# Kernel optimization log

Measured on AMD Instinct MI355X. Metric: run time of the kernel, lower is better.

## Reference

```python
import jax, jax.numpy as jnp
import numpy as np

N_NODES = 40000
N_EDGES = 640000
NFEAT = 256
NHID = 128


def setup_inputs() -> dict:
    key = jax.random.key(0)
    k1, k2, k3, k4 = jax.random.split(key, 4)
    x = jax.random.normal(k1, (N_NODES, NFEAT), dtype=jnp.float32)
    edge_index = jax.random.randint(k2, (2, N_EDGES), 0, N_NODES, dtype=jnp.int64)
    edge_weight = jax.random.uniform(k3, (N_EDGES,), dtype=jnp.float32)
    # Glorot-style init for the GraphConvolution weight, zero bias
    W = jax.random.normal(k4, (NFEAT, NHID), dtype=jnp.float32) * (1.0 / np.sqrt(NFEAT))
    b = jnp.zeros((NHID,), dtype=jnp.float32)
    return {"x": x, "edge_index": edge_index, "edge_weight": edge_weight, "W": W, "b": b}


def reference(x, edge_index, edge_weight, W, b):
    # GraphConvolution: support = x @ W ; out = spmm(adj, support) + b ; relu
    support = x @ W                                   # [N, nhid]
    src, dst = edge_index[0], edge_index[1]
    msgs = support[src] * edge_weight[:, None]        # [E, nhid] gathered messages
    agg = jax.ops.segment_sum(msgs, dst, num_segments=N_NODES)  # [N, nhid]
    return jax.nn.relu(agg + b)
```

## Files before the change

kernel.cpp:

```cpp
#include <hip/hip_runtime.h>

#define NNODES 40000
#define NEDGES 640000
#define NFEAT  256
#define NHID   128
#define CAP    48

#define SUP_OFF 0u
#define CUR_OFF 10240000u
#define WT_OFF  10400000u
#define BKT_OFF 10465536u
#define WS_NEEDED (BKT_OFF + (size_t)NNODES * CAP * 4)

#define GEMM_BLOCKS (NNODES / 64)
#define FILL_BLOCKS (NEDGES / 1024)

typedef float floatx4 __attribute__((ext_vector_type(4)));
typedef __bf16 bf16x8 __attribute__((ext_vector_type(8)));
typedef unsigned short ushort8 __attribute__((ext_vector_type(8)));
union BfFrag { ushort8 s; bf16x8 b; };

__device__ __forceinline__ unsigned short f2bf(float f) {
    unsigned int u = __float_as_uint(f);
    u = (u + 0x7FFFu + ((u >> 16) & 1u)) >> 16;
    return (unsigned short)u;
}

__device__ __forceinline__ float4 bf4(unsigned int lo, unsigned int hi) {
    float4 v;
    v.x = __uint_as_float(lo << 16);
    v.y = __uint_as_float(lo & 0xFFFF0000u);
    v.z = __uint_as_float(hi << 16);
    v.w = __uint_as_float(hi & 0xFFFF0000u);
    return v;
}

__global__ __launch_bounds__(256) void setup_wt_cur(const float* __restrict__ W,
                                                    unsigned short* __restrict__ Wt,
                                                    int* __restrict__ cursor) {
    const int i = blockIdx.x * 256 + threadIdx.x;
    if (i < NNODES) cursor[i] = 0;
    if (i < NFEAT * NHID) {
        const int h = i >> 8;
        const int k = i & 255;
        Wt[i] = f2bf(W[k * NHID + h]);
    }
}

__global__ __launch_bounds__(256) void gemm_fill(const float* __restrict__ x,
                                                 const unsigned short* __restrict__ Wt,
                                                 unsigned short* __restrict__ support,
                                                 const int* __restrict__ ei,
                                                 const float* __restrict__ ew,
                                                 int* __restrict__ cursor,
                                                 unsigned int* __restrict__ bucket) {
    const int tid = threadIdx.x;

    if (blockIdx.x >= GEMM_BLOCKS) {
        const int base = (blockIdx.x - GEMM_BLOCKS) * 1024 + tid;

        int src[4], dst[4];
        float w[4];
        #pragma unroll
        for (int j = 0; j < 4; j++) {
            const int e = base + j * 256;
            src[j] = ei[e];
            dst[j] = ei[NEDGES + e];
            w[j]   = ew[e];
        }

        int pos[4];
        #pragma unroll
        for (int j = 0; j < 4; j++)
            pos[j] = atomicAdd(&cursor[dst[j]], 1);

        #pragma unroll
        for (int j = 0; j < 4; j++) {
            const unsigned int entry =
                ((unsigned int)f2bf(w[j]) << 16) | (unsigned int)src[j];
            if (pos[j] < CAP)
                bucket[(size_t)dst[j] * CAP + pos[j]] = entry;
        }
        return;
    }

    const int lane = tid & 63;
    const int wv   = tid >> 6;
    const int m    = lane & 15;
    const int quad = lane >> 4;
    const int node = blockIdx.x * 64 + wv * 16 + m;

    BfFrag afrag[8];
    const float* xrow = x + (size_t)node * NFEAT + quad * 8;
    #pragma unroll
    for (int ks = 0; ks < 8; ks++) {
        float4 f0 = *(const float4*)(xrow + ks * 32);
        float4 f1 = *(const float4*)(xrow + ks * 32 + 4);
        afrag[ks].s[0] = f2bf(f0.x); afrag[ks].s[1] = f2bf(f0.y);
        afrag[ks].s[2] = f2bf(f0.z); afrag[ks].s[3] = f2bf(f0.w);
        afrag[ks].s[4] = f2bf(f1.x); afrag[ks].s[5] = f2bf(f1.y);
        afrag[ks].s[6] = f2bf(f1.z); afrag[ks].s[7] = f2bf(f1.w);
    }

    floatx4 acc[8];
    #pragma unroll
    for (int nt = 0; nt < 8; nt++) acc[nt] = (floatx4){0.f, 0.f, 0.f, 0.f};

    #pragma unroll
    for (int nt = 0; nt < 8; nt++) {
        const unsigned short* wrow = Wt + (size_t)(nt * 16 + m) * NFEAT + quad * 8;
        #pragma unroll
        for (int ks = 0; ks < 8; ks++) {
            BfFrag bfrag;
            bfrag.s = *(const ushort8*)(wrow + ks * 32);
            acc[nt] = __builtin_amdgcn_mfma_f32_16x16x32_bf16(afrag[ks].b, bfrag.b,
                                                              acc[nt], 0, 0, 0);
        }
    }

    const int row0 = blockIdx.x * 64 + wv * 16 + quad * 4;
    #pragma unroll
    for (int nt = 0; nt < 8; nt++) {
        #pragma unroll
        for (int r = 0; r < 4; r++) {
            support[(size_t)(row0 + r) * NHID + nt * 16 + m] = f2bf(acc[nt][r]);
        }
    }
}

__global__ __launch_bounds__(256) void gather_csr(const int* __restrict__ cursor,
                                                  const unsigned int* __restrict__ bucket,
                                                  const unsigned short* __restrict__ support,
                                                  const float* __restrict__ b,
                                                  float* __restrict__ out) {
    const int node = blockIdx.x * 4 + (threadIdx.x >> 6);
    const int lane = threadIdx.x & 63;
    const int q    = lane >> 4;
    const int ql   = lane & 15;

    int cnt = cursor[node];
    if (cnt > CAP) cnt = CAP;
    const unsigned int* bkt  = bucket + (size_t)node * CAP;
    const uint4*        sup4 = (const uint4*)support;

    float4 lo0 = make_float4(0.f, 0.f, 0.f, 0.f), lo1 = lo0, lo2 = lo0, lo3 = lo0;
    float4 hi0 = lo0, hi1 = lo0, hi2 = lo0, hi3 = lo0;

    int i = 0;
    for (; i + 16 <= cnt; i += 16) {
        unsigned int e0 = bkt[i + 0  + q];
        unsigned int e1 = bkt[i + 4  + q];
        unsigned int e2 = bkt[i + 8  + q];
        unsigned int e3 = bkt[i + 12 + q];
        uint4 u0 = sup4[(size_t)(e0 & 0xFFFFu) * 16 + ql];
        uint4 u1 = sup4[(size_t)(e1 & 0xFFFFu) * 16 + ql];
        uint4 u2 = sup4[(size_t)(e2 & 0xFFFFu) * 16 + ql];
        uint4 u3 = sup4[(size_t)(e3 & 0xFFFFu) * 16 + ql];
        float w0 = __uint_as_float(e0 & 0xFFFF0000u);
        float w1 = __uint_as_float(e1 & 0xFFFF0000u);
        float w2 = __uint_as_float(e2 & 0xFFFF0000u);
        float w3 = __uint_as_float(e3 & 0xFFFF0000u);
        float4 vl0 = bf4(u0.x, u0.y), vh0 = bf4(u0.z, u0.w);
        float4 vl1 = bf4(u1.x, u1.y), vh1 = bf4(u1.z, u1.w);
        float4 vl2 = bf4(u2.x, u2.y), vh2 = bf4(u2.z, u2.w);
        float4 vl3 = bf4(u3.x, u3.y), vh3 = bf4(u3.z, u3.w);
        lo0.x = fmaf(w0, vl0.x, lo0.x); lo0.y = fmaf(w0, vl0.y, lo0.y);
        lo0.z = fmaf(w0, vl0.z, lo0.z); lo0.w = fmaf(w0, vl0.w, lo0.w);
        hi0.x = fmaf(w0, vh0.x, hi0.x); hi0.y = fmaf(w0, vh0.y, hi0.y);
        hi0.z = fmaf(w0, vh0.z, hi0.z); hi0.w = fmaf(w0, vh0.w, hi0.w);
        lo1.x = fmaf(w1, vl1.x, lo1.x); lo1.y = fmaf(w1, vl1.y, lo1.y);
        lo1.z = fmaf(w1, vl1.z, lo1.z); lo1.w = fmaf(w1, vl1.w, lo1.w);
        hi1.x = fmaf(w1, vh1.x, hi1.x); hi1.y = fmaf(w1, vh1.y, hi1.y);
        hi1.z = fmaf(w1, vh1.z, hi1.z); hi1.w = fmaf(w1, vh1.w, hi1.w);
        lo2.x = fmaf(w2, vl2.x, lo2.x); lo2.y = fmaf(w2, vl2.y, lo2.y);
        lo2.z = fmaf(w2, vl2.z, lo2.z); lo2.w = fmaf(w2, vl2.w, lo2.w);
        hi2.x = fmaf(w2, vh2.x, hi2.x); hi2.y = fmaf(w2, vh2.y, hi2.y);
        hi2.z = fmaf(w2, vh2.z, hi2.z); hi2.w = fmaf(w2, vh2.w, hi2.w);
        lo3.x = fmaf(w3, vl3.x, lo3.x); lo3.y = fmaf(w3, vl3.y, lo3.y);
        lo3.z = fmaf(w3, vl3.z, lo3.z); lo3.w = fmaf(w3, vl3.w, lo3.w);
        hi3.x = fmaf(w3, vh3.x, hi3.x); hi3.y = fmaf(w3, vh3.y, hi3.y);
        hi3.z = fmaf(w3, vh3.z, hi3.z); hi3.w = fmaf(w3, vh3.w, hi3.w);
    }

    if (i < cnt) {
        #pragma unroll
        for (int j = 0; j < 4; j++) {
            int e = i + 4 * j + q;
            bool valid = e < cnt;
            unsigned int ent = bkt[valid ? e : 0];
            float w = valid ? __uint_as_float(ent & 0xFFFF0000u) : 0.f;
            uint4 u = sup4[(size_t)(ent & 0xFFFFu) * 16 + ql];
            float4 vl = bf4(u.x, u.y), vh = bf4(u.z, u.w);
            lo0.x = fmaf(w, vl.x, lo0.x); lo0.y = fmaf(w, vl.y, lo0.y);
            lo0.z = fmaf(w, vl.z, lo0.z); lo0.w = fmaf(w, vl.w, lo0.w);
            hi0.x = fmaf(w, vh.x, hi0.x); hi0.y = fmaf(w, vh.y, hi0.y);
            hi0.z = fmaf(w, vh.z, hi0.z); hi0.w = fmaf(w, vh.w, hi0.w);
        }
    }

    float4 L, H;
    L.x = (lo0.x + lo1.x) + (lo2.x + lo3.x);
    L.y = (lo0.y + lo1.y) + (lo2.y + lo3.y);
    L.z = (lo0.z + lo1.z) + (lo2.z + lo3.z);
    L.w = (lo0.w + lo1.w) + (lo2.w + lo3.w);
    H.x = (hi0.x + hi1.x) + (hi2.x + hi3.x);
    H.y = (hi0.y + hi1.y) + (hi2.y + hi3.y);
    H.z = (hi0.z + hi1.z) + (hi2.z + hi3.z);
    H.w = (hi0.w + hi1.w) + (hi2.w + hi3.w);

    L.x += __shfl_xor(L.x, 16); L.y += __shfl_xor(L.y, 16);
    L.z += __shfl_xor(L.z, 16); L.w += __shfl_xor(L.w, 16);
    H.x += __shfl_xor(H.x, 16); H.y += __shfl_xor(H.y, 16);
    H.z += __shfl_xor(H.z, 16); H.w += __shfl_xor(H.w, 16);
    L.x += __shfl_xor(L.x, 32); L.y += __shfl_xor(L.y, 32);
    L.z += __shfl_xor(L.z, 32); L.w += __shfl_xor(L.w, 32);
    H.x += __shfl_xor(H.x, 32); H.y += __shfl_xor(H.y, 32);
    H.z += __shfl_xor(H.z, 32); H.w += __shfl_xor(H.w, 32);

    if (q == 0) {
        const float4* b4p = (const float4*)b;
        float4 bl = b4p[ql * 2], bh = b4p[ql * 2 + 1];
        L.x = fmaxf(L.x + bl.x, 0.f); L.y = fmaxf(L.y + bl.y, 0.f);
        L.z = fmaxf(L.z + bl.z, 0.f); L.w = fmaxf(L.w + bl.w, 0.f);
        H.x = fmaxf(H.x + bh.x, 0.f); H.y = fmaxf(H.y + bh.y, 0.f);
        H.z = fmaxf(H.z + bh.z, 0.f); H.w = fmaxf(H.w + bh.w, 0.f);
        float4* o4 = (float4*)out + (size_t)node * (NHID / 4);
        o4[ql * 2]     = L;
        o4[ql * 2 + 1] = H;
    }
}

__global__ __launch_bounds__(256) void gemm_xw(const float* __restrict__ x,
                                               const float* __restrict__ W,
                                               float* __restrict__ support) {
    __shared__ float xs[64 * NFEAT];
    const int tid   = threadIdx.x;
    const int node0 = blockIdx.x * 64;

    const float4* xg  = (const float4*)(x + (size_t)node0 * NFEAT);
    float4*       xs4 = (float4*)xs;
    #pragma unroll
    for (int i = tid; i < 64 * (NFEAT / 4); i += 256) xs4[i] = xg[i];
    __syncthreads();

    const int hg = tid & 31;
    const int ng = tid >> 5;
    const float4* W4 = (const float4*)W;

    float4 acc[8];
    #pragma unroll
    for (int n = 0; n < 8; n++) acc[n] = make_float4(0.f, 0.f, 0.f, 0.f);

    #pragma unroll 4
    for (int k = 0; k < NFEAT; k++) {
        float4 w = W4[k * (NHID / 4) + hg];
        #pragma unroll
        for (int n = 0; n < 8; n++) {
            float xv = xs[(ng * 8 + n) * NFEAT + k];
            acc[n].x = fmaf(xv, w.x, acc[n].x);
            acc[n].y = fmaf(xv, w.y, acc[n].y);
            acc[n].z = fmaf(xv, w.z, acc[n].z);
            acc[n].w = fmaf(xv, w.w, acc[n].w);
        }
    }

    float4* out4 = (float4*)support;
    #pragma unroll
    for (int n = 0; n < 8; n++)
        out4[(size_t)(node0 + ng * 8 + n) * (NHID / 4) + hg] = acc[n];
}

__global__ __launch_bounds__(256) void scatter_edges(const int* __restrict__ ei,
                                                     const float* __restrict__ ew,
                                                     const float* __restrict__ support,
                                                     float* __restrict__ out) {
    const int tid  = threadIdx.x;
    const int lane = tid & 31;
    const int e    = blockIdx.x * 8 + (tid >> 5);
    const int   src = ei[e];
    const int   dst = ei[NEDGES + e];
    const float w   = ew[e];
    const float4* s4 = (const float4*)support;
    float4 v = s4[(size_t)src * (NHID / 4) + lane];
    float* o = out + (size_t)dst * NHID + lane * 4;
    atomicAdd(o + 0, v.x * w);
    atomicAdd(o + 1, v.y * w);
    atomicAdd(o + 2, v.z * w);
    atomicAdd(o + 3, v.w * w);
}

__global__ __launch_bounds__(256) void finalize(float* __restrict__ out,
                                                const float* __restrict__ b) {
    const int i = blockIdx.x * 256 + threadIdx.x;
    float4*       o4 = (float4*)out;
    const float4* b4 = (const float4*)b;
    float4 v  = o4[i];
    float4 bb = b4[i & 31];
    v.x = fmaxf(v.x + bb.x, 0.f);
    v.y = fmaxf(v.y + bb.y, 0.f);
    v.z = fmaxf(v.z + bb.z, 0.f);
    v.w = fmaxf(v.w + bb.w, 0.f);
    o4[i] = v;
}

extern "C" void kernel_launch(void* const* d_in, const int* in_sizes, int n_in,
                              void* d_out, int out_size, void* d_ws, size_t ws_size,
                              hipStream_t stream) {
    const float* x  = (const float*)d_in[0];
    const int*   ei = (const int*)d_in[1];
    const float* ew = (const float*)d_in[2];
    const float* W  = (const float*)d_in[3];
    const float* b  = (const float*)d_in[4];
    float*       out = (float*)d_out;

    char* ws = (char*)d_ws;

    if (ws_size >= WS_NEEDED) {
        unsigned short* support = (unsigned short*)(ws + SUP_OFF);
        int*            cursor  = (int*)(ws + CUR_OFF);
        unsigned short* Wt      = (unsigned short*)(ws + WT_OFF);
        unsigned int*   bucket  = (unsigned int*)(ws + BKT_OFF);

        setup_wt_cur<<<160, 256, 0, stream>>>(W, Wt, cursor);
        gemm_fill<<<GEMM_BLOCKS + FILL_BLOCKS, 256, 0, stream>>>(
            x, Wt, support, ei, ew, cursor, bucket);
        gather_csr<<<NNODES / 4, 256, 0, stream>>>(cursor, bucket, support, b, out);
    } else {
        float* support = (float*)(ws + SUP_OFF);
        gemm_xw<<<NNODES / 64, 256, 0, stream>>>(x, W, support);
        hipMemsetAsync(d_out, 0, (size_t)out_size * sizeof(float), stream);
        scatter_edges<<<NEDGES / 8, 256, 0, stream>>>(ei, ew, support, out);
        finalize<<<out_size / 4 / 256, 256, 0, stream>>>(out, b);
    }
}
```

Before: 156.6 us.

## Partition bucket-fill atomics into 8 node classes and launch fill blocks first

The edge-bucketing part of the fused GEMM+fill kernel is restructured. Each fill block now handles one of 8 node classes (dst & 7) over a slice of edges, and the cursor array is re-laid out so each class owns a contiguous region. The goal is to localize atomic traffic, likely so it stays within one XCD/L2 slice, and the fill blocks are scheduled ahead of the GEMM blocks. In exchange, every fill block reads 8x more edge data (each edge is read by all 8 class blocks), and the gather kernel looks up cursors through a remapped index.

```diff
diff --git a/kernel.cpp b/kernel.cpp
--- a/kernel.cpp
+++ b/kernel.cpp
@@ -13,7 +13,10 @@
 #define WS_NEEDED (BKT_OFF + (size_t)NNODES * CAP * 4)
 
 #define GEMM_BLOCKS (NNODES / 64)
-#define FILL_BLOCKS (NEDGES / 1024)
+#define FILLB   1000
+#define SLICES  (FILLB / 8)
+#define EPSL    (NEDGES / SLICES)
+#define NPERP   (NNODES / 8)
 
 typedef float floatx4 __attribute__((ext_vector_type(4)));
 typedef __bf16 bf16x8 __attribute__((ext_vector_type(8)));
@@ -25,6 +28,8 @@
     u = (u + 0x7FFFu + ((u >> 16) & 1u)) >> 16;
     return (unsigned short)u;
 }
+
+__device__ __forceinline__ int cidx(int n) { return (n & 7) * NPERP + (n >> 3); }
 
 __device__ __forceinline__ float4 bf4(unsigned int lo, unsigned int hi) {
     float4 v;
@@ -56,39 +61,50 @@
                                                  unsigned int* __restrict__ bucket) {
     const int tid = threadIdx.x;
 
-    if (blockIdx.x >= GEMM_BLOCKS) {
-        const int base = (blockIdx.x - GEMM_BLOCKS) * 1024 + tid;
-
-        int src[4], dst[4];
-        float w[4];
-        #pragma unroll
-        for (int j = 0; j < 4; j++) {
-            const int e = base + j * 256;
-            src[j] = ei[e];
-            dst[j] = ei[NEDGES + e];
-            w[j]   = ew[e];
-        }
-
-        int pos[4];
-        #pragma unroll
-        for (int j = 0; j < 4; j++)
-            pos[j] = atomicAdd(&cursor[dst[j]], 1);
-
-        #pragma unroll
-        for (int j = 0; j < 4; j++) {
-            const unsigned int entry =
-                ((unsigned int)f2bf(w[j]) << 16) | (unsigned int)src[j];
-            if (pos[j] < CAP)
-                bucket[(size_t)dst[j] * CAP + pos[j]] = entry;
+    if (blockIdx.x < FILLB) {
+        const int p = blockIdx.x & 7;
+        const int s = blockIdx.x >> 3;
+        int* __restrict__ curp = cursor + p * NPERP;
+        const int base = s * EPSL + tid;
+
+        #pragma unroll 1
+        for (int bq = 0; bq < EPSL / 1024; bq++) {
+            int src[4], dst[4];
+            float w[4];
+            #pragma unroll
+            for (int j = 0; j < 4; j++) {
+                const int e = base + bq * 1024 + j * 256;
+                src[j] = ei[e];
+                dst[j] = ei[NEDGES + e];
+                w[j]   = ew[e];
+            }
+
+            bool act[4];
+            int pos[4];
+            #pragma unroll
+            for (int j = 0; j < 4; j++) {
+                act[j] = (dst[j] & 7) == p;
+                pos[j] = act[j] ? atomicAdd(&curp[dst[j] >> 3], 1) : CAP;
+            }
+
+            #pragma unroll
+            for (int j = 0; j < 4; j++) {
+                if (act[j] && pos[j] < CAP) {
+                    const unsigned int entry =
+                        ((unsigned int)f2bf(w[j]) << 16) | (unsigned int)src[j];
+                    bucket[(size_t)dst[j] * CAP + pos[j]] = entry;
+                }
+            }
         }
         return;
     }
 
+    const int gb   = blockIdx.x - FILLB;
     const int lane = tid & 63;
     const int wv   = tid >> 6;
     const int m    = lane & 15;
     const int quad = lane >> 4;
-    const int node = blockIdx.x * 64 + wv * 16 + m;
+    const int node = gb * 64 + wv * 16 + m;
 
     BfFrag afrag[8];
     const float* xrow = x + (size_t)node * NFEAT + quad * 8;
@@ -118,7 +134,7 @@
         }
     }
 
-    const int row0 = blockIdx.x * 64 + wv * 16 + quad * 4;
+    const int row0 = gb * 64 + wv * 16 + quad * 4;
     #pragma unroll
     for (int nt = 0; nt < 8; nt++) {
         #pragma unroll
@@ -138,7 +154,7 @@
     const int q    = lane >> 4;
     const int ql   = lane & 15;
 
-    int cnt = cursor[node];
+    int cnt = cursor[cidx(node)];
     if (cnt > CAP) cnt = CAP;
     const unsigned int* bkt  = bucket + (size_t)node * CAP;
     const uint4*        sup4 = (const uint4*)support;
@@ -322,7 +338,7 @@
         unsigned int*   bucket  = (unsigned int*)(ws + BKT_OFF);
 
         setup_wt_cur<<<160, 256, 0, stream>>>(W, Wt, cursor);
-        gemm_fill<<<GEMM_BLOCKS + FILL_BLOCKS, 256, 0, stream>>>(
+        gemm_fill<<<FILLB + GEMM_BLOCKS, 256, 0, stream>>>(
             x, Wt, support, ei, ew, cursor, bucket);
         gather_csr<<<NNODES / 4, 256, 0, stream>>>(cursor, bucket, support, b, out);
     } else {
```

Result: slower. 168.6 us (+7.7%).

## Fuse setup, GEMM/fill and gather into one cooperative persistent kernel

Applied to the files above, without the earlier changes.

Replaces the three-kernel sequence (setup, GEMM+bucket fill, CSR gather) with a single cooperative-launched persistent kernel that uses grid-wide syncs between phases. Blocks are statically split between edge-bucket filling and bf16 MFMA GEMM work in the middle phase, then all blocks grid-stride over node groups for the gather. This is meant to remove kernel launch gaps and tail effects. In exchange it adds grid.sync overhead, caps occupancy to what is co-resident, and relies on a fixed fill/GEMM block ratio that may leave one side idle.

```diff
diff --git a/kernel.cpp b/kernel.cpp
--- a/kernel.cpp
+++ b/kernel.cpp
@@ -1,4 +1,7 @@
 #include <hip/hip_runtime.h>
+#include <hip/hip_cooperative_groups.h>
+
+namespace cg = cooperative_groups;
 
 #define NNODES 40000
 #define NEDGES 640000
@@ -12,8 +15,9 @@
 #define BKT_OFF 10465536u
 #define WS_NEEDED (BKT_OFF + (size_t)NNODES * CAP * 4)
 
-#define GEMM_BLOCKS (NNODES / 64)
-#define FILL_BLOCKS (NEDGES / 1024)
+#define NCHUNK     625
+#define GEMM_UNITS 625
+#define NGROUPS    (NNODES / 4)
 
 typedef float floatx4 __attribute__((ext_vector_type(4)));
 typedef __bf16 bf16x8 __attribute__((ext_vector_type(8)));
@@ -34,6 +38,208 @@
     v.w = __uint_as_float(hi & 0xFFFF0000u);
     return v;
 }
+
+__global__ __launch_bounds__(256, 4) void fused_gcn(
+        const float* __restrict__ x,
+        const int* __restrict__ ei,
+        const float* __restrict__ ew,
+        const float* __restrict__ W,
+        const float* __restrict__ b,
+        float* __restrict__ out,
+        unsigned short* __restrict__ support,
+        int* __restrict__ cursor,
+        unsigned short* __restrict__ Wt,
+        unsigned int* __restrict__ bucket,
+        int nfill) {
+    cg::grid_group grid = cg::this_grid();
+    const int tid  = threadIdx.x;
+    const int bid  = blockIdx.x;
+    const int nblk = gridDim.x;
+
+    for (int i = bid * 256 + tid; i < NNODES; i += nblk * 256) {
+        cursor[i] = 0;
+        if (i < NFEAT * NHID) {
+            const int h = i >> 8;
+            const int k = i & 255;
+            Wt[i] = f2bf(W[k * NHID + h]);
+        }
+    }
+    __threadfence();
+    grid.sync();
+
+    if (bid < nfill) {
+        for (int c = bid; c < NCHUNK; c += nfill) {
+            const int base = c * 1024 + tid;
+            int src[4], dst[4];
+            float w[4];
+            #pragma unroll
+            for (int j = 0; j < 4; j++) {
+                const int e = base + j * 256;
+                src[j] = ei[e];
+                dst[j] = ei[NEDGES + e];
+                w[j]   = ew[e];
+            }
+            int pos[4];
+            #pragma unroll
+            for (int j = 0; j < 4; j++) pos[j] = atomicAdd(&cursor[dst[j]], 1);
+            #pragma unroll
+            for (int j = 0; j < 4; j++) {
+                if (pos[j] < CAP)
+                    bucket[(size_t)dst[j] * CAP + pos[j]] =
+                        ((unsigned int)f2bf(w[j]) << 16) | (unsigned int)src[j];
+            }
+        }
+    } else {
+        for (int gb = bid - nfill; gb < GEMM_UNITS; gb += nblk - nfill) {
+            const int lane = tid & 63;
+            const int wv   = tid >> 6;
+            const int m    = lane & 15;
+            const int quad = lane >> 4;
+            const int node = gb * 64 + wv * 16 + m;
+
+            BfFrag afrag[8];
+            const float* xrow = x + (size_t)node * NFEAT + quad * 8;
+            #pragma unroll
+            for (int ks = 0; ks < 8; ks++) {
+                float4 f0 = *(const float4*)(xrow + ks * 32);
+                float4 f1 = *(const float4*)(xrow + ks * 32 + 4);
+                afrag[ks].s[0] = f2bf(f0.x); afrag[ks].s[1] = f2bf(f0.y);
+                afrag[ks].s[2] = f2bf(f0.z); afrag[ks].s[3] = f2bf(f0.w);
+                afrag[ks].s[4] = f2bf(f1.x); afrag[ks].s[5] = f2bf(f1.y);
+                afrag[ks].s[6] = f2bf(f1.z); afrag[ks].s[7] = f2bf(f1.w);
+            }
+
+            floatx4 acc[8];
+            #pragma unroll
+            for (int nt = 0; nt < 8; nt++) acc[nt] = (floatx4){0.f, 0.f, 0.f, 0.f};
+
+            #pragma unroll
+            for (int nt = 0; nt < 8; nt++) {
+                const unsigned short* wrow = Wt + (size_t)(nt * 16 + m) * NFEAT + quad * 8;
+                #pragma unroll
+                for (int ks = 0; ks < 8; ks++) {
+                    BfFrag bfrag;
+                    bfrag.s = *(const ushort8*)(wrow + ks * 32);
+                    acc[nt] = __builtin_amdgcn_mfma_f32_16x16x32_bf16(afrag[ks].b, bfrag.b,
+                                                                      acc[nt], 0, 0, 0);
+                }
+            }
+
+            const int row0 = gb * 64 + wv * 16 + quad * 4;
+            #pragma unroll
+            for (int nt = 0; nt < 8; nt++) {
+                #pragma unroll
+                for (int r = 0; r < 4; r++) {
+                    support[(size_t)(row0 + r) * NHID + nt * 16 + m] = f2bf(acc[nt][r]);
+                }
+            }
+        }
+    }
+    __threadfence();
+    grid.sync();
+
+    const int lane = tid & 63;
+    const int q    = lane >> 4;
+    const int ql   = lane & 15;
+    const uint4* sup4 = (const uint4*)support;
+
+    for (int g = bid; g < NGROUPS; g += nblk) {
+        const int node = g * 4 + (tid >> 6);
+
+        int cnt = cursor[node];
+        if (cnt > CAP) cnt = CAP;
+        const unsigned int* bkt = bucket + (size_t)node * CAP;
+
+        float4 lo0 = make_float4(0.f, 0.f, 0.f, 0.f), lo1 = lo0, lo2 = lo0, lo3 = lo0;
+        float4 hi0 = lo0, hi1 = lo0, hi2 = lo0, hi3 = lo0;
+
+        int i = 0;
+        for (; i + 16 <= cnt; i += 16) {
+            unsigned int e0 = bkt[i + 0  + q];
+            unsigned int e1 = bkt[i + 4  + q];
+            unsigned int e2 = bkt[i + 8  + q];
+            unsigned int e3 = bkt[i + 12 + q];
+            uint4 u0 = sup4[(size_t)(e0 & 0xFFFFu) * 16 + ql];
+            uint4 u1 = sup4[(size_t)(e1 & 0xFFFFu) * 16 + ql];
+            uint4 u2 = sup4[(size_t)(e2 & 0xFFFFu) * 16 + ql];
+            uint4 u3 = sup4[(size_t)(e3 & 0xFFFFu) * 16 + ql];
+            float w0 = __uint_as_float(e0 & 0xFFFF0000u);
+            float w1 = __uint_as_float(e1 & 0xFFFF0000u);
+            float w2 = __uint_as_float(e2 & 0xFFFF0000u);
+            float w3 = __uint_as_float(e3 & 0xFFFF0000u);
+            float4 vl0 = bf4(u0.x, u0.y), vh0 = bf4(u0.z, u0.w);
+            float4 vl1 = bf4(u1.x, u1.y), vh1 = bf4(u1.z, u1.w);
+            float4 vl2 = bf4(u2.x, u2.y), vh2 = bf4(u2.z, u2.w);
+            float4 vl3 = bf4(u3.x, u3.y), vh3 = bf4(u3.z, u3.w);
+            lo0.x = fmaf(w0, vl0.x, lo0.x); lo0.y = fmaf(w0, vl0.y, lo0.y);
+            lo0.z = fmaf(w0, vl0.z, lo0.z); lo0.w = fmaf(w0, vl0.w, lo0.w);
+            hi0.x = fmaf(w0, vh0.x, hi0.x); hi0.y = fmaf(w0, vh0.y, hi0.y);
+            hi0.z = fmaf(w0, vh0.z, hi0.z); hi0.w = fmaf(w0, vh0.w, hi0.w);
+            lo1.x = fmaf(w1, vl1.x, lo1.x); lo1.y = fmaf(w1, vl1.y, lo1.y);
+            lo1.z = fmaf(w1, vl1.z, lo1.z); lo1.w = fmaf(w1, vl1.w, lo1.w);
+            hi1.x = fmaf(w1, vh1.x, hi1.x); hi1.y = fmaf(w1, vh1.y, hi1.y);
+            hi1.z = fmaf(w1, vh1.z, hi1.z); hi1.w = fmaf(w1, vh1.w, hi1.w);
+            lo2.x = fmaf(w2, vl2.x, lo2.x); lo2.y = fmaf(w2, vl2.y, lo2.y);
+            lo2.z = fmaf(w2, vl2.z, lo2.z); lo2.w = fmaf(w2, vl2.w, lo2.w);
+            hi2.x = fmaf(w2, vh2.x, hi2.x); hi2.y = fmaf(w2, vh2.y, hi2.y);
+            hi2.z = fmaf(w2, vh2.z, hi2.z); hi2.w = fmaf(w2, vh2.w, hi2.w);
+            lo3.x = fmaf(w3, vl3.x, lo3.x); lo3.y = fmaf(w3, vl3.y, lo3.y);
+            lo3.z = fmaf(w3, vl3.z, lo3.z); lo3.w = fmaf(w3, vl3.w, lo3.w);
+            hi3.x = fmaf(w3, vh3.x, hi3.x); hi3.y = fmaf(w3, vh3.y, hi3.y);
+            hi3.z = fmaf(w3, vh3.z, hi3.z); hi3.w = fmaf(w3, vh3.w, hi3.w);
+        }
+
+        if (i < cnt) {
+            #pragma unroll
+            for (int j = 0; j < 4; j++) {
+                int e = i + 4 * j + q;
+                bool valid = e < cnt;
+                unsigned int ent = bkt[valid ? e : 0];
+                float w = valid ? __uint_as_float(ent & 0xFFFF0000u) : 0.f;
+                uint4 u = sup4[(size_t)(ent & 0xFFFFu) * 16 + ql];
+                float4 vl = bf4(u.x, u.y), vh = bf4(u.z, u.w);
+                lo0.x = fmaf(w, vl.x, lo0.x); lo0.y = fmaf(w, vl.y, lo0.y);
+                lo0.z = fmaf(w, vl.z, lo0.z); lo0.w = fmaf(w, vl.w, lo0.w);
+                hi0.x = fmaf(w, vh.x, hi0.x); hi0.y = fmaf(w, vh.y, hi0.y);
+                hi0.z = fmaf(w, vh.z, hi0.z); hi0.w = fmaf(w, vh.w, hi0.w);
+            }
+        }
+
+        float4 L, H;
+        L.x = (lo0.x + lo1.x) + (lo2.x + lo3.x);
+        L.y = (lo0.y + lo1.y) + (lo2.y + lo3.y);
+        L.z = (lo0.z + lo1.z) + (lo2.z + lo3.z);
+        L.w = (lo0.w + lo1.w) + (lo2.w + lo3.w);
+        H.x = (hi0.x + hi1.x) + (hi2.x + hi3.x);
+        H.y = (hi0.y + hi1.y) + (hi2.y + hi3.y);
+        H.z = (hi0.z + hi1.z) + (hi2.z + hi3.z);
+        H.w = (hi0.w + hi1.w) + (hi2.w + hi3.w);
+
+        L.x += __shfl_xor(L.x, 16); L.y += __shfl_xor(L.y, 16);
+        L.z += __shfl_xor(L.z, 16); L.w += __shfl_xor(L.w, 16);
+        H.x += __shfl_xor(H.x, 16); H.y += __shfl_xor(H.y, 16);
+        H.z += __shfl_xor(H.z, 16); H.w += __shfl_xor(H.w, 16);
+        L.x += __shfl_xor(L.x, 32); L.y += __shfl_xor(L.y, 32);
+        L.z += __shfl_xor(L.z, 32); L.w += __shfl_xor(L.w, 32);
+        H.x += __shfl_xor(H.x, 32); H.y += __shfl_xor(H.y, 32);
+        H.z += __shfl_xor(H.z, 32); H.w += __shfl_xor(H.w, 32);
+
+        if (q == 0) {
+            const float4* b4p = (const float4*)b;
+            float4 bl = b4p[ql * 2], bh = b4p[ql * 2 + 1];
+            L.x = fmaxf(L.x + bl.x, 0.f); L.y = fmaxf(L.y + bl.y, 0.f);
+            L.z = fmaxf(L.z + bl.z, 0.f); L.w = fmaxf(L.w + bl.w, 0.f);
+            H.x = fmaxf(H.x + bh.x, 0.f); H.y = fmaxf(H.y + bh.y, 0.f);
+            H.z = fmaxf(H.z + bh.z, 0.f); H.w = fmaxf(H.w + bh.w, 0.f);
+            float4* o4 = (float4*)out + (size_t)node * (NHID / 4);
+            o4[ql * 2]     = L;
+            o4[ql * 2 + 1] = H;
+        }
+    }
+}
+
+#define GEMM_BLOCKS (NNODES / 64)
+#define FILL_BLOCKS (NEDGES / 1024)
 
 __global__ __launch_bounds__(256) void setup_wt_cur(const float* __restrict__ W,
                                                     unsigned short* __restrict__ Wt,
@@ -58,7 +264,6 @@
 
     if (blockIdx.x >= GEMM_BLOCKS) {
         const int base = (blockIdx.x - GEMM_BLOCKS) * 1024 + tid;
-
         int src[4], dst[4];
         float w[4];
         #pragma unroll
@@ -68,12 +273,9 @@
             dst[j] = ei[NEDGES + e];
             w[j]   = ew[e];
         }
-
         int pos[4];
         #pragma unroll
-        for (int j = 0; j < 4; j++)
-            pos[j] = atomicAdd(&cursor[dst[j]], 1);
-
+        for (int j = 0; j < 4; j++) pos[j] = atomicAdd(&cursor[dst[j]], 1);
         #pragma unroll
         for (int j = 0; j < 4; j++) {
             const unsigned int entry =
@@ -321,10 +523,38 @@
         unsigned short* Wt      = (unsigned short*)(ws + WT_OFF);
         unsigned int*   bucket  = (unsigned int*)(ws + BKT_OFF);
 
-        setup_wt_cur<<<160, 256, 0, stream>>>(W, Wt, cursor);
-        gemm_fill<<<GEMM_BLOCKS + FILL_BLOCKS, 256, 0, stream>>>(
-            x, Wt, support, ei, ew, cursor, bucket);
-        gather_csr<<<NNODES / 4, 256, 0, stream>>>(cursor, bucket, support, b, out);
+        static int gridSize = -1;
+        if (gridSize < 0) {
+            int coopAttr = 0, dev = 0;
+            hipGetDevice(&dev);
+            hipDeviceGetAttribute(&coopAttr, hipDeviceAttributeCooperativeLaunch, dev);
+            int occ = 0;
+            hipError_t oe = hipOccupancyMaxActiveBlocksPerMultiprocessor(
+                &occ, (const void*)fused_gcn, 256, 0);
+            gridSize = (coopAttr && oe == hipSuccess && occ > 0) ? occ * 256 : 0;
+            if (gridSize > 2048) gridSize = 2048;
+        }
+
+        bool launched = false;
+        if (gridSize >= 256) {
+            int nfill = (gridSize * 2) / 5;
+            if (nfill < 1) nfill = 1;
+            void* args[] = {(void*)&x, (void*)&ei, (void*)&ew, (void*)&W,
+                            (void*)&b, (void*)&out, (void*)&support,
+                            (void*)&cursor, (void*)&Wt, (void*)&bucket,
+                            (void*)&nfill};
+            hipError_t le = hipLaunchCooperativeKernel((void*)fused_gcn,
+                                                       dim3(gridSize), dim3(256),
+                                                       args, 0, stream);
+            launched = (le == hipSuccess);
+        }
+
+        if (!launched) {
+            setup_wt_cur<<<160, 256, 0, stream>>>(W, Wt, cursor);
+            gemm_fill<<<GEMM_BLOCKS + FILL_BLOCKS, 256, 0, stream>>>(
+                x, Wt, support, ei, ew, cursor, bucket);
+            gather_csr<<<NNODES / 4, 256, 0, stream>>>(cursor, bucket, support, b, out);
+        }
     } else {
         float* support = (float*)(ws + SUP_OFF);
         gemm_xw<<<NNODES / 64, 256, 0, stream>>>(x, W, support);
```

New measurement: 474.4 us. 3.03x slower.
